# Kernel tuning notes

Hardware: AMD Instinct MI355X
Metric: run time of the kernel (lower is better)

Reference implementation:

```python
import jax, jax.numpy as jnp
import numpy as np

N_EMBD = 768
N_HEAD = 12
HEAD_SIZE = N_EMBD // N_HEAD  # 64
WINDOW = 64  # sliding_window_size
EPS = 1e-6


def _rmsnorm(x, g):
    xf = x.astype(jnp.float32)
    n = xf * jax.lax.rsqrt(jnp.mean(xf * xf, axis=-1, keepdims=True) + EPS)
    return n.astype(x.dtype) * g


def _gelu_tanh(x):
    c = jnp.sqrt(jnp.asarray(2.0 / jnp.pi, x.dtype))
    return 0.5 * x * (1.0 + jnp.tanh(c * (x + 0.044715 * x ** 3)))


def setup_inputs() -> dict:
    key = jax.random.key(0)
    ks = jax.random.split(key, 12)
    B, T = 8, 1024
    s = 0.02
    return {
        "x": jax.random.normal(ks[0], (B, T, N_EMBD), jnp.float32),
        "w_q": jax.random.normal(ks[1], (N_EMBD, N_HEAD, HEAD_SIZE), jnp.float32) * s,
        "w_k": jax.random.normal(ks[2], (N_EMBD, N_HEAD, HEAD_SIZE), jnp.float32) * s,
        "w_v": jax.random.normal(ks[3], (N_EMBD, N_HEAD, HEAD_SIZE), jnp.float32) * s,
        "w_proj": jax.random.normal(ks[4], (N_EMBD, N_EMBD), jnp.float32) * s,
        "b_proj": jnp.zeros((N_EMBD,), jnp.float32),
        "w_ff1": jax.random.normal(ks[5], (N_EMBD, 4 * N_EMBD), jnp.float32) * s,
        "b_ff1": jnp.zeros((4 * N_EMBD,), jnp.float32),
        "w_ff2": jax.random.normal(ks[6], (4 * N_EMBD, N_EMBD), jnp.float32) * s,
        "b_ff2": jnp.zeros((N_EMBD,), jnp.float32),
        "g1": jnp.ones((N_EMBD,), jnp.float32),
        "g2": jnp.ones((N_EMBD,), jnp.float32),
    }


def reference(x, w_q, w_k, w_v, w_proj, b_proj, w_ff1, b_ff1, w_ff2, b_ff2, g1, g2):
    B, T, C = x.shape
    # ---- multi-head sliding-window causal attention (eval: dropout = identity) ----
    h = _rmsnorm(x, g1)
    q = jnp.einsum("btc,chd->bhtd", h, w_q)
    k = jnp.einsum("btc,chd->bhtd", h, w_k)
    v = jnp.einsum("btc,chd->bhtd", h, w_v)
    scores = jnp.einsum("bhtd,bhsd->bhts", q, k) / jnp.sqrt(jnp.asarray(HEAD_SIZE, x.dtype))
    pos = jnp.arange(T)
    diff = pos[:, None] - pos[None, :]  # q_pos - k_pos
    mask = (diff < 0) | (diff >= WINDOW)  # causal + sliding window of 64
    scores = jnp.where(mask[None, None], jnp.asarray(-jnp.inf, scores.dtype), scores)
    attn = jax.nn.softmax(scores, axis=-1)
    out = jnp.einsum("bhts,bhsd->bhtd", attn, v)
    out = out.transpose(0, 2, 1, 3).reshape(B, T, C)  # concat heads
    x = x + out @ w_proj + b_proj
    # ---- feedforward ----
    h2 = _rmsnorm(x, g2)
    ff = _gelu_tanh(h2 @ w_ff1 + b_ff1) @ w_ff2 + b_ff2
    x = x + ff
    aux = jnp.asarray(0.0, jnp.float32)
    return (x, aux)
```

## Files before the change

kernel.cpp:

```cpp
#include <hip/hip_runtime.h>
#include <cstdint>

#define DEVI __device__ __forceinline__

typedef __bf16 bf16x8 __attribute__((ext_vector_type(8)));
typedef float  f32x4  __attribute__((ext_vector_type(4)));

template<int V> struct IC { static constexpr int v = V; };

DEVI unsigned short f2b(float f){
  unsigned u = __builtin_bit_cast(unsigned, f);
  unsigned r = u + 0x7FFF + ((u >> 16) & 1);
  return (unsigned short)(r >> 16);
}
DEVI float b2f(unsigned short s){
  unsigned u = ((unsigned)s) << 16;
  return __builtin_bit_cast(float, u);
}
DEVI float gelu_f(float x){
  float u = 0.7978845608028654f * (x + 0.044715f * x * x * x);
  float e = __expf(2.0f * u);
  return x * (1.0f - 1.0f / (e + 1.0f));
}
DEVI void gl_lds16(const unsigned short* g, unsigned short* l){
  __builtin_amdgcn_global_load_lds(
      (const __attribute__((address_space(1))) unsigned int*)g,
      (__attribute__((address_space(3))) unsigned int*)l, 16, 0, 0);
}

__global__ __launch_bounds__(256)
void transpose_all(const float* __restrict__ w_q, const float* __restrict__ w_k,
                   const float* __restrict__ w_v, const float* __restrict__ w_proj,
                   const float* __restrict__ w_ff1, const float* __restrict__ w_ff2,
                   unsigned short* __restrict__ WqkvT, unsigned short* __restrict__ WprojT,
                   unsigned short* __restrict__ Wff1T, unsigned short* __restrict__ Wff2T)
{
  __shared__ float tile[32][33];
  int blk = blockIdx.x;
  const float* in; unsigned short* out; int R, C, b0;
  if      (blk < 576) { in = w_q;    out = WqkvT;              R = 768;  C = 768;  b0 = 0;    }
  else if (blk < 1152){ in = w_k;    out = WqkvT + 768 * 768;  R = 768;  C = 768;  b0 = 576;  }
  else if (blk < 1728){ in = w_v;    out = WqkvT + 1536 * 768; R = 768;  C = 768;  b0 = 1152; }
  else if (blk < 2304){ in = w_proj; out = WprojT;             R = 768;  C = 768;  b0 = 1728; }
  else if (blk < 4608){ in = w_ff1;  out = Wff1T;              R = 768;  C = 3072; b0 = 2304; }
  else                { in = w_ff2;  out = Wff2T;              R = 3072; C = 768;  b0 = 4608; }
  int lb = blk - b0;
  int nbx = C >> 5;
  int bx = lb % nbx, by = lb / nbx;
  int c0 = bx << 5, r0 = by << 5;
  int tx = threadIdx.x & 31, ty = threadIdx.x >> 5;
  #pragma unroll
  for (int j = 0; j < 32; j += 8)
    tile[ty + j][tx] = in[(size_t)(r0 + ty + j) * C + c0 + tx];
  __syncthreads();
  #pragma unroll
  for (int j = 0; j < 32; j += 8)
    out[(size_t)(c0 + ty + j) * R + r0 + tx] = f2b(tile[tx][ty + j]);
}

__global__ __launch_bounds__(256)
void rmsnorm_k(const float* __restrict__ x, const float* __restrict__ g,
               unsigned short* __restrict__ out)
{
  int wid = threadIdx.x >> 6, lane = threadIdx.x & 63;
  size_t row = (size_t)blockIdx.x * 4 + wid;
  const float* xr = x + row * 768;
  float4 v[3];
  float ss = 0.0f;
  #pragma unroll
  for (int c = 0; c < 3; c++){
    v[c] = *(const float4*)&xr[lane * 4 + c * 256];
    ss += v[c].x * v[c].x + v[c].y * v[c].y + v[c].z * v[c].z + v[c].w * v[c].w;
  }
  #pragma unroll
  for (int o = 32; o >= 1; o >>= 1) ss += __shfl_xor(ss, o);
  float rs = rsqrtf(ss * (1.0f / 768.0f) + 1e-6f);
  #pragma unroll
  for (int c = 0; c < 3; c++){
    const float4 gv = *(const float4*)&g[lane * 4 + c * 256];
    ushort4 o4;
    o4.x = f2b(v[c].x * rs * gv.x);
    o4.y = f2b(v[c].y * rs * gv.y);
    o4.z = f2b(v[c].z * rs * gv.z);
    o4.w = f2b(v[c].w * rs * gv.w);
    *(ushort4*)&out[row * 768 + lane * 4 + c * 256] = o4;
  }
}

template<int TPB, bool BIAS, bool GELU_, bool RES, bool OUTF32>
__global__ __launch_bounds__(256, 3)
void gemm_db(const unsigned short* __restrict__ A, const unsigned short* __restrict__ Bt,
             const float* __restrict__ bias, const float* __restrict__ res,
             void* __restrict__ outp, int M, int N, int K)
{
  constexpr int BM = 64;
  constexpr int MI = 2;
  constexpr int AL = 2;
  constexpr int BUFSZ = (BM + 128) * 64;
  __shared__ unsigned short sm[2][BUFSZ];

  int tid = threadIdx.x, wid = tid >> 6, lane = tid & 63;
  int la = lane & 15, hi = lane >> 4;
  int wm = wid >> 1, wn = wid & 1;
  int tiles_n = N >> 7;
  int bid = blockIdx.x;
  bid = (bid & 7) * (gridDim.x >> 3) + (bid >> 3);
  int g0 = bid * TPB;
  int NT = K >> 6;

  size_t constA[AL]; unsigned short* aDst[2][AL];
  size_t constB[4];  unsigned short* bDst[2][4];
  #pragma unroll
  for (int l = 0; l < AL; l++){
    int cb = wid * (BM * 2) + l * 64;
    int idx = cb + lane;
    int row = idx >> 3, sl2 = (idx & 7) ^ (row & 7);
    constA[l] = (size_t)row * K + sl2 * 8;
    aDst[0][l] = &sm[0][cb * 8];
    aDst[1][l] = &sm[1][cb * 8];
  }
  #pragma unroll
  for (int l = 0; l < 4; l++){
    int cb = wid * 256 + l * 64;
    int idx = cb + lane;
    int row = idx >> 3, sl2 = (idx & 7) ^ (row & 7);
    constB[l] = (size_t)row * K + sl2 * 8;
    bDst[0][l] = &sm[0][BM * 64 + cb * 8];
    bDst[1][l] = &sm[1][BM * 64 + cb * 8];
  }

  const unsigned short* fa[2][2];
  const unsigned short* fb[2][2];
  #pragma unroll
  for (int bf = 0; bf < 2; bf++)
    #pragma unroll
    for (int kk = 0; kk < 2; kk++){
      int sw = (((kk * 4 + hi) ^ (la & 7))) * 8;
      fa[bf][kk] = &sm[bf][(wm * (BM / 2) + la) * 64 + sw];
      fb[bf][kk] = &sm[bf][BM * 64 + (wn * 64 + la) * 64 + sw];
    }

  const unsigned short* aSrc[AL];
  const unsigned short* bSrc[4];
  auto setSrc = [&](int g){
    int m0 = (g / tiles_n) * BM, n0 = (g % tiles_n) << 7;
    #pragma unroll
    for (int l = 0; l < AL; l++) aSrc[l] = A  + (size_t)m0 * K + constA[l];
    #pragma unroll
    for (int l = 0; l < 4;  l++) bSrc[l] = Bt + (size_t)n0 * K + constB[l];
  };
  auto stageTo = [&](auto BF){
    constexpr int bf = decltype(BF)::v;
    #pragma unroll
    for (int l = 0; l < AL; l++){ gl_lds16(aSrc[l], aDst[bf][l]); aSrc[l] += 64; }
    #pragma unroll
    for (int l = 0; l < 4; l++){ gl_lds16(bSrc[l], bDst[bf][l]); bSrc[l] += 64; }
  };

  setSrc(g0);
  stageTo(IC<0>{});

  float* outF = (float*)outp;
  unsigned short* outB = (unsigned short*)outp;

  for (int ot = 0; ot < TPB; ot++){
    int g = g0 + ot;
    int m0 = (g / tiles_n) * BM, n0 = (g % tiles_n) << 7;

    f32x4 acc[MI][4] = {};

    auto tile_step = [&](auto BUF, int t){
      constexpr int CB = decltype(BUF)::v;
      if (t + 1 < NT || ot + 1 < TPB){
        if (t + 1 == NT) setSrc(g + 1);
        stageTo(IC<CB ^ 1>{});
        asm volatile("s_waitcnt vmcnt(6)" ::: "memory");
      } else {
        asm volatile("s_waitcnt vmcnt(0)" ::: "memory");
      }
      __builtin_amdgcn_s_barrier();

      bf16x8 afr[MI][2], bfr[4][2];
      #pragma unroll
      for (int mm = 0; mm < MI; mm++){
        afr[mm][0] = *(const bf16x8*)(fa[CB][0] + mm * 1024);
        afr[mm][1] = *(const bf16x8*)(fa[CB][1] + mm * 1024);
      }
      #pragma unroll
      for (int nn = 0; nn < 4; nn++){
        bfr[nn][0] = *(const bf16x8*)(fb[CB][0] + nn * 1024);
        bfr[nn][1] = *(const bf16x8*)(fb[CB][1] + nn * 1024);
      }
      __builtin_amdgcn_s_setprio(1);
      #pragma unroll
      for (int mm = 0; mm < MI; mm++)
        #pragma unroll
        for (int nn = 0; nn < 4; nn++)
          #pragma unroll
          for (int kk = 0; kk < 2; kk++)
            acc[mm][nn] = __builtin_amdgcn_mfma_f32_16x16x32_bf16(
                afr[mm][kk], bfr[nn][kk], acc[mm][nn], 0, 0, 0);
      __builtin_amdgcn_s_setprio(0);

      __builtin_amdgcn_s_barrier();
    };

    for (int t = 0; t < NT; t += 2){
      tile_step(IC<0>{}, t);
      tile_step(IC<1>{}, t + 1);
    }

    #pragma unroll
    for (int mm = 0; mm < MI; mm++){
      int rowb = m0 + wm * (BM / 2) + mm * 16 + hi * 4;
      #pragma unroll
      for (int nn = 0; nn < 4; nn++){
        int col = n0 + wn * 64 + nn * 16 + la;
        float bv = BIAS ? bias[col] : 0.0f;
        #pragma unroll
        for (int r = 0; r < 4; r++){
          float val = acc[mm][nn][r] + bv;
          if (GELU_) val = gelu_f(val);
          if (RES)   val += res[(size_t)(rowb + r) * N + col];
          size_t o = (size_t)(rowb + r) * N + col;
          if (OUTF32) outF[o] = val;
          else        outB[o] = f2b(val);
        }
      }
    }
  }
}

__global__ __launch_bounds__(256)
void attn_k(const unsigned short* __restrict__ qkv, unsigned short* __restrict__ attn)
{
  __shared__ unsigned short Qs[64 * 72];
  __shared__ unsigned short Ks[128 * 72];
  __shared__ unsigned short Vt[64 * 136];
  __shared__ unsigned short Ps[4][16 * 136];

  int tid = threadIdx.x, wid = tid >> 6, lane = tid & 63;
  int la = lane & 15, hi = lane >> 4;
  int blk = blockIdx.x;
  blk = (blk & 7) * (gridDim.x >> 3) + (blk >> 3);
  int tile = blk & 15, hb = blk >> 4;
  int h = hb % 12, b = hb / 12;
  int t0 = tile << 6;

  const unsigned short* qbase = qkv + (size_t)(b * 1024) * 2304 + h * 64;

  #pragma unroll
  for (int r = 0; r < 2; r++){
    int idx = tid + r * 256;
    int row = idx >> 3, ch = idx & 7;
    uint4 v = *(const uint4*)(qbase + (size_t)(t0 + row) * 2304 + ch * 8);
    *(uint4*)&Qs[row * 72 + ch * 8] = v;
  }
  #pragma unroll
  for (int r = 0; r < 4; r++){
    int idx = tid + r * 256;
    int row = idx >> 3, ch = idx & 7;
    int sg = t0 - 64 + row; sg = sg < 0 ? 0 : sg;
    uint4 v = *(const uint4*)(qbase + 768 + (size_t)sg * 2304 + ch * 8);
    *(uint4*)&Ks[row * 72 + ch * 8] = v;
  }
  #pragma unroll
  for (int r = 0; r < 4; r++){
    int idx = tid + r * 256;
    int s = idx & 127, ch = idx >> 7;
    int sg = t0 - 64 + s; sg = sg < 0 ? 0 : sg;
    uint4 v = *(const uint4*)(qbase + 1536 + (size_t)sg * 2304 + ch * 8);
    unsigned short tmp[8];
    *(uint4*)tmp = v;
    #pragma unroll
    for (int j = 0; j < 8; j++)
      Vt[(ch * 8 + j) * 136 + s] = tmp[j];
  }
  __syncthreads();

  f32x4 sc[8];
  #pragma unroll
  for (int sj = 0; sj < 8; sj++) sc[sj] = (f32x4){0.f, 0.f, 0.f, 0.f};
  #pragma unroll
  for (int kk = 0; kk < 2; kk++){
    bf16x8 aq = *(const bf16x8*)&Qs[(wid * 16 + la) * 72 + kk * 32 + hi * 8];
    #pragma unroll
    for (int sj = 0; sj < 8; sj++){
      bf16x8 bk = *(const bf16x8*)&Ks[(sj * 16 + la) * 72 + kk * 32 + hi * 8];
      sc[sj] = __builtin_amdgcn_mfma_f32_16x16x32_bf16(aq, bk, sc[sj], 0, 0, 0);
    }
  }

  float inv[4];
  #pragma unroll
  for (int r2 = 0; r2 < 4; r2++){
    int row = wid * 16 + hi * 4 + r2;
    float mx = -1e30f;
    #pragma unroll
    for (int sj = 0; sj < 8; sj++){
      int sl = sj * 16 + la;
      bool valid = (sl >= row + 1) && (sl <= row + 64) && (t0 - 64 + sl >= 0);
      float sv = valid ? sc[sj][r2] * 0.125f : -1e30f;
      sc[sj][r2] = sv;
      mx = fmaxf(mx, sv);
    }
    #pragma unroll
    for (int o = 8; o >= 1; o >>= 1) mx = fmaxf(mx, __shfl_xor(mx, o));
    float sum = 0.0f;
    #pragma unroll
    for (int sj = 0; sj < 8; sj++){
      float p = __expf(sc[sj][r2] - mx);
      sc[sj][r2] = p;
      sum += p;
    }
    #pragma unroll
    for (int o = 8; o >= 1; o >>= 1) sum += __shfl_xor(sum, o);
    inv[r2] = 1.0f / sum;
  }

  unsigned short* myP = Ps[wid];
  #pragma unroll
  for (int sj = 0; sj < 8; sj++)
    #pragma unroll
    for (int r2 = 0; r2 < 4; r2++)
      myP[(hi * 4 + r2) * 136 + sj * 16 + la] = f2b(sc[sj][r2]);

  __syncthreads();

  f32x4 oacc[4];
  #pragma unroll
  for (int nj = 0; nj < 4; nj++) oacc[nj] = (f32x4){0.f, 0.f, 0.f, 0.f};
  #pragma unroll
  for (int ks = 0; ks < 4; ks++){
    bf16x8 ap = *(const bf16x8*)&myP[la * 136 + ks * 32 + hi * 8];
    #pragma unroll
    for (int nj = 0; nj < 4; nj++){
      bf16x8 bv = *(const bf16x8*)&Vt[(nj * 16 + la) * 136 + ks * 32 + hi * 8];
      oacc[nj] = __builtin_amdgcn_mfma_f32_16x16x32_bf16(ap, bv, oacc[nj], 0, 0, 0);
    }
  }

  unsigned short* obase = attn + (size_t)(b * 1024 + t0) * 768 + h * 64;
  #pragma unroll
  for (int nj = 0; nj < 4; nj++)
    #pragma unroll
    for (int r2 = 0; r2 < 4; r2++){
      int row = wid * 16 + hi * 4 + r2;
      obase[(size_t)row * 768 + nj * 16 + la] = f2b(oacc[nj][r2] * inv[r2]);
    }
}

__global__ void aux_k(float* p){ if (threadIdx.x == 0) p[0] = 0.0f; }

extern "C" void kernel_launch(void* const* d_in, const int* in_sizes, int n_in,
                              void* d_out, int out_size, void* d_ws, size_t ws_size,
                              hipStream_t stream)
{
  const float* x      = (const float*)d_in[0];
  const float* w_q    = (const float*)d_in[1];
  const float* w_k    = (const float*)d_in[2];
  const float* w_v    = (const float*)d_in[3];
  const float* w_proj = (const float*)d_in[4];
  const float* b_proj = (const float*)d_in[5];
  const float* w_ff1  = (const float*)d_in[6];
  const float* b_ff1  = (const float*)d_in[7];
  const float* w_ff2  = (const float*)d_in[8];
  const float* b_ff2  = (const float*)d_in[9];
  const float* g1     = (const float*)d_in[10];
  const float* g2     = (const float*)d_in[11];
  float* out = (float*)d_out;

  char* ws = (char*)d_ws;
  size_t off = 0;
  auto alloc = [&](size_t bytes){ size_t r = off; off += (bytes + 255) & ~(size_t)255; return r; };
  const size_t BT = 8 * 1024;

  unsigned short* h     = (unsigned short*)(ws + alloc(BT * 768 * 2));
  unsigned short* qkv   = (unsigned short*)(ws + alloc(BT * 3072 * 2));
  float*          x2    = (float*)         (ws + alloc(BT * 768 * 4));
  unsigned short* h2    = (unsigned short*)(ws + alloc(BT * 768 * 2));
  unsigned short* WqkvT = (unsigned short*)(ws + alloc(2304 * 768 * 2));
  unsigned short* WprojT= (unsigned short*)(ws + alloc(768 * 768 * 2));
  unsigned short* Wff1T = (unsigned short*)(ws + alloc(3072 * 768 * 2));
  unsigned short* Wff2T = (unsigned short*)(ws + alloc(768 * 3072 * 2));
  unsigned short* attn  = h;
  unsigned short* ffa   = qkv;

  transpose_all<<<6912, 256, 0, stream>>>(w_q, w_k, w_v, w_proj, w_ff1, w_ff2,
                                          WqkvT, WprojT, Wff1T, Wff2T);

  rmsnorm_k<<<2048, 256, 0, stream>>>(x, g1, h);

  gemm_db<3,false,false,false,false><<<768, 256, 0, stream>>>(h, WqkvT, nullptr, nullptr, qkv, 8192, 2304, 768);

  attn_k<<<8 * 12 * 16, 256, 0, stream>>>(qkv, attn);

  gemm_db<1,true,false,true,true><<<768, 256, 0, stream>>>(attn, WprojT, b_proj, x, x2, 8192, 768, 768);

  rmsnorm_k<<<2048, 256, 0, stream>>>(x2, g2, h2);

  gemm_db<4,true,true,false,false><<<768, 256, 0, stream>>>(h2, Wff1T, b_ff1, nullptr, ffa, 8192, 3072, 768);

  gemm_db<1,true,false,true,true><<<768, 256, 0, stream>>>(ffa, Wff2T, b_ff2, x2, out, 8192, 768, 3072);

  aux_k<<<1, 64, 0, stream>>>(out + 6291456);
}
```

Baseline: 208.8 us.

## Add 32x32x16 MFMA GEMM kernel with two-block occupancy for FF1

Adds a new persistent GEMM kernel that uses the 32x32x16 bf16 MFMA instruction instead of 16x16 tiles, with a double-buffered LDS pipeline, launch bounds allowing two blocks per CU, and s_setprio around the MFMA bursts. The FF1 GEMM (with bias and GELU) switches to it, with 512 blocks each covering 3 output tiles instead of 768 blocks covering 4. The aim is higher MFMA throughput per LDS read and better latency hiding. The risk is register pressure from 64 accumulator floats per lane and a scattered epilogue store pattern.

```diff
diff --git a/kernel.cpp b/kernel.cpp
--- a/kernel.cpp
+++ b/kernel.cpp
@@ -5,6 +5,7 @@
 
 typedef __bf16 bf16x8 __attribute__((ext_vector_type(8)));
 typedef float  f32x4  __attribute__((ext_vector_type(4)));
+typedef float  f32x16 __attribute__((ext_vector_type(16)));
 
 template<int V> struct IC { static constexpr int v = V; };
 
@@ -231,6 +232,141 @@
   }
 }
 
+template<int TPB, bool BIAS, bool GELU_, bool OUTF32>
+__global__ __launch_bounds__(256, 2)
+void gemm32(const unsigned short* __restrict__ A, const unsigned short* __restrict__ Bt,
+            const float* __restrict__ bias, void* __restrict__ outp,
+            int M, int N, int K)
+{
+  __shared__ unsigned short sm[2][16384];
+  int tid = threadIdx.x, wid = tid >> 6, lane = tid & 63;
+  int l31 = lane & 31, hi2 = lane >> 5;
+  int wm = wid >> 1, wn = wid & 1;
+  int tiles_n = N >> 7;
+  int bid = blockIdx.x;
+  bid = (bid & 7) * (gridDim.x >> 3) + (bid >> 3);
+  int g0 = bid * TPB;
+  int NT = K >> 6;
+
+  f32x16 acc[2][2];
+
+  size_t constA[4], constB[4];
+  #pragma unroll
+  for (int l = 0; l < 4; l++){
+    int cb = wid * 256 + l * 64;
+    int idx = cb + lane;
+    int row = idx >> 3, sl2 = (idx & 7) ^ (row & 7);
+    constA[l] = (size_t)row * K + sl2 * 8;
+    constB[l] = (size_t)row * K + sl2 * 8;
+  }
+
+  int aRow = (wm * 64 + l31) * 64;
+  int bRow = (wn * 64 + l31) * 64;
+  int swk[4];
+  #pragma unroll
+  for (int ks = 0; ks < 4; ks++)
+    swk[ks] = (((ks * 2 + hi2) ^ (l31 & 7))) * 8;
+
+  const unsigned short* aSrc[4];
+  const unsigned short* bSrc[4];
+  auto setSrc = [&](int g){
+    int m0 = (g / tiles_n) << 7, n0 = (g % tiles_n) << 7;
+    #pragma unroll
+    for (int l = 0; l < 4; l++){
+      aSrc[l] = A  + (size_t)m0 * K + constA[l];
+      bSrc[l] = Bt + (size_t)n0 * K + constB[l];
+    }
+  };
+  auto stageTo = [&](auto BF){
+    constexpr int bf = decltype(BF)::v;
+    #pragma unroll
+    for (int l = 0; l < 4; l++){
+      gl_lds16(aSrc[l], &sm[bf][wid * 2048 + l * 512]);        aSrc[l] += 64;
+    }
+    #pragma unroll
+    for (int l = 0; l < 4; l++){
+      gl_lds16(bSrc[l], &sm[bf][8192 + wid * 2048 + l * 512]); bSrc[l] += 64;
+    }
+  };
+
+  setSrc(g0);
+  stageTo(IC<0>{});
+
+  float* outF = (float*)outp;
+  unsigned short* outB = (unsigned short*)outp;
+
+  for (int ot = 0; ot < TPB; ot++){
+    int g = g0 + ot;
+    int m0 = (g / tiles_n) << 7, n0 = (g % tiles_n) << 7;
+
+    #pragma unroll
+    for (int mi = 0; mi < 2; mi++)
+      #pragma unroll
+      for (int nn = 0; nn < 2; nn++)
+        acc[mi][nn] = (f32x16){};
+
+    auto tile_step = [&](auto BUF, int t){
+      constexpr int CB = decltype(BUF)::v;
+      if (t + 1 < NT || ot + 1 < TPB){
+        if (t + 1 == NT) setSrc(g + 1);
+        stageTo(IC<CB ^ 1>{});
+        asm volatile("s_waitcnt vmcnt(8)" ::: "memory");
+      } else {
+        asm volatile("s_waitcnt vmcnt(0)" ::: "memory");
+      }
+      __builtin_amdgcn_s_barrier();
+
+      const unsigned short* As = sm[CB];
+      const unsigned short* Bs = sm[CB] + 8192;
+      bf16x8 av[2][4], bv[2][4];
+      #pragma unroll
+      for (int ks = 0; ks < 4; ks++){
+        #pragma unroll
+        for (int mi = 0; mi < 2; mi++)
+          av[mi][ks] = *(const bf16x8*)&As[aRow + mi * 2048 + swk[ks]];
+        #pragma unroll
+        for (int nn = 0; nn < 2; nn++)
+          bv[nn][ks] = *(const bf16x8*)&Bs[bRow + nn * 2048 + swk[ks]];
+      }
+      __builtin_amdgcn_s_setprio(1);
+      #pragma unroll
+      for (int ks = 0; ks < 4; ks++)
+        #pragma unroll
+        for (int mi = 0; mi < 2; mi++)
+          #pragma unroll
+          for (int nn = 0; nn < 2; nn++)
+            acc[mi][nn] = __builtin_amdgcn_mfma_f32_32x32x16_bf16(
+                av[mi][ks], bv[nn][ks], acc[mi][nn], 0, 0, 0);
+      __builtin_amdgcn_s_setprio(0);
+
+      __builtin_amdgcn_s_barrier();
+    };
+
+    for (int t = 0; t < NT; t += 2){
+      tile_step(IC<0>{}, t);
+      tile_step(IC<1>{}, t + 1);
+    }
+
+    #pragma unroll
+    for (int mi = 0; mi < 2; mi++){
+      #pragma unroll
+      for (int nn = 0; nn < 2; nn++){
+        int col = n0 + wn * 64 + nn * 32 + l31;
+        float bvs = BIAS ? bias[col] : 0.0f;
+        #pragma unroll
+        for (int reg = 0; reg < 16; reg++){
+          int row = m0 + wm * 64 + mi * 32 + (reg & 3) + 8 * (reg >> 2) + 4 * hi2;
+          float val = acc[mi][nn][reg] + bvs;
+          if (GELU_) val = gelu_f(val);
+          size_t o = (size_t)row * N + col;
+          if (OUTF32) outF[o] = val;
+          else        outB[o] = f2b(val);
+        }
+      }
+    }
+  }
+}
+
 __global__ __launch_bounds__(256)
 void attn_k(const unsigned short* __restrict__ qkv, unsigned short* __restrict__ attn)
 {
@@ -399,7 +535,7 @@
 
   rmsnorm_k<<<2048, 256, 0, stream>>>(x2, g2, h2);
 
-  gemm_db<4,true,true,false,false><<<768, 256, 0, stream>>>(h2, Wff1T, b_ff1, nullptr, ffa, 8192, 3072, 768);
+  gemm32<3,true,true,false><<<512, 256, 0, stream>>>(h2, Wff1T, b_ff1, ffa, 8192, 3072, 768);
 
   gemm_db<1,true,false,true,true><<<768, 256, 0, stream>>>(ffa, Wff2T, b_ff2, x2, out, 8192, 768, 3072);
 
```

New measurement: 208.2 us. Within noise of the previous version (-0.3%).
